# Kernel optimization log

Measured on AMD Instinct MI355X. Metric: run time of the kernel, lower is better.

Reference implementation:

```python
import jax, jax.numpy as jnp
import numpy as np

B, H, S, D = 2, 16, 2048, 128
ALIBI_MAX_BIAS = 8.0


def alibi_bias(seq_len: int, num_heads: int):
    # slopes = 2 ** -(start, 2*start, ..., num_heads*start), start = max_bias / num_heads
    start = ALIBI_MAX_BIAS / num_heads
    slopes = jnp.exp2(-(jnp.arange(1, num_heads + 1, dtype=jnp.float32) * start))  # [H]
    dist = (jnp.arange(seq_len)[None, :] - jnp.arange(seq_len)[:, None]).astype(jnp.float32)  # [S,S] j-i
    return (dist[None, :, :] * slopes[:, None, None])[None]  # [1,H,S,S]


def setup_inputs() -> dict:
    key = jax.random.key(0)
    kq, kk, kv = jax.random.split(key, 3)
    q = jax.random.normal(kq, (B, H, S, D), dtype=jnp.float32)
    k = jax.random.normal(kk, (B, H, S, D), dtype=jnp.float32)
    v = jax.random.normal(kv, (B, H, S, D), dtype=jnp.float32)
    mask = jnp.tril(jnp.ones((S, S), dtype=jnp.int32))[None, None]  # causal [1,1,S,S]
    return {"q": q, "k": k, "v": v, "mask": mask}


def reference(q, k, v, mask):
    dim = q.shape[-1]
    scale = jnp.sqrt(jnp.asarray(dim, dtype=q.dtype))
    alibi = alibi_bias(k.shape[-2], k.shape[-3]).astype(q.dtype)
    mat = jnp.einsum("bhsd,bhtd->bhst", q, k) / scale + alibi  # [B,H,S,S]
    mat = jnp.where(mask == 0, jnp.asarray(-1000000.0, dtype=mat.dtype), mat)
    mat = jax.nn.softmax(mat, axis=-1)
    return jnp.einsum("bhst,bhtd->bhsd", mat, v)
```

## Files before the change

### kernel.cpp

```cpp
#include <hip/hip_runtime.h>
#include <hip/hip_bf16.h>

typedef short s16x8 __attribute__((ext_vector_type(8)));
typedef float f32x16 __attribute__((ext_vector_type(16)));

#define LOG2E 1.44269504088896f

__device__ __forceinline__ unsigned bfpack2(float lo, float hi) {
  unsigned a = (unsigned)__builtin_bit_cast(unsigned short, __float2bfloat16(lo));
  unsigned b = (unsigned)__builtin_bit_cast(unsigned short, __float2bfloat16(hi));
  return a | (b << 16);
}

union U4 { unsigned u[4]; uint4 q; s16x8 v; };

__global__ __launch_bounds__(128)
void prep_kv(const float* __restrict__ Kg, const float* __restrict__ Vg,
             char* __restrict__ tiles) {
  constexpr int S = 2048, Dh = 128;
  const int g  = (int)blockIdx.x;
  const int bh = g >> 6, t = g & 63;
  const size_t base = (size_t)bh * S * Dh + (size_t)(t << 5) * Dh;
  char* out = tiles + ((size_t)g << 14);
  const int tid = (int)threadIdx.x;
  const int lane = tid & 63, half = tid >> 6;
  const int l31 = lane & 31, h5 = lane >> 5;

  {
    const float* krow = Kg + base + (size_t)l31 * Dh;
    #pragma unroll
    for (int i = 0; i < 4; ++i) {
      const int ks = half * 4 + i;
      const float* p = krow + 16 * ks + 8 * h5;
      float4 a = *(const float4*)p;
      float4 b = *(const float4*)(p + 4);
      U4 w;
      w.u[0] = bfpack2(a.x, a.y); w.u[1] = bfpack2(a.z, a.w);
      w.u[2] = bfpack2(b.x, b.y); w.u[3] = bfpack2(b.z, b.w);
      *(uint4*)(out + ks * 1024 + lane * 16) = w.q;
    }
  }
  __shared__ float lds[32][132];
  {
    const int rv = tid >> 2, q4 = tid & 3;
    const float* vrow = Vg + base + (size_t)rv * Dh;
    #pragma unroll
    for (int p = 0; p < 8; ++p)
      *(float4*)(&lds[rv][q4 * 4 + p * 16]) = *(const float4*)(vrow + q4 * 4 + p * 16);
  }
  __syncthreads();
  {
    #pragma unroll
    for (int i = 0; i < 4; ++i) {
      const int gp = half * 4 + i;
      const int ks = gp >> 2, dt = gp & 3;
      const int cv = 2 * ks + h5, d = 32 * dt + l31;
      U4 w;
      #pragma unroll
      for (int u = 0; u < 4; ++u)
        w.u[u] = bfpack2(lds[8 * cv + 2 * u][d], lds[8 * cv + 2 * u + 1][d]);
      *(uint4*)(out + 8192 + gp * 1024 + lane * 16) = w.q;
    }
  }
}

__global__ __launch_bounds__(128, 2)
void attn_alibi(const float* __restrict__ Qg, float* __restrict__ Og,
                const char* __restrict__ tiles) {
  constexpr int S = 2048, Dh = 128;
  const int lid  = (int)blockIdx.x;
  const int xcd  = lid & 7;
  const int r8   = lid >> 3;
  const int bh   = xcd + 8 * (r8 & 3);
  const int qt   = 63 - (r8 >> 2);
  const int head = bh & 15;

  const int tid  = (int)threadIdx.x;
  const int wq   = tid >> 6;
  const int lane = tid & 63, l31 = lane & 31, h5 = lane >> 5;

  const float c1     = 0.08838834764831845f * LOG2E;
  const float slope2 = exp2f(-0.5f * (float)(head + 1)) * LOG2E;

  const char* tb = tiles + (((size_t)bh << 6) << 14);

  float cpat[16];
  #pragma unroll
  for (int r = 0; r < 16; ++r)
    cpat[r] = slope2 * (float)((r & 3) + 8 * (r >> 2) + 4 * h5);

  __shared__ float olds[4][64][17];
  __shared__ float mlds[2][2][32];

  const int iq = (qt << 5) + l31;

  s16x8 qf[8];
  {
    const float* qrow = Qg + (size_t)bh * S * Dh + (size_t)iq * Dh;
    #pragma unroll
    for (int ks = 0; ks < 8; ++ks) {
      const float* p = qrow + 16 * ks + 8 * h5;
      float4 a = *(const float4*)p;
      float4 b = *(const float4*)(p + 4);
      U4 w;
      w.u[0] = bfpack2(a.x, a.y); w.u[1] = bfpack2(a.z, a.w);
      w.u[2] = bfpack2(b.x, b.y); w.u[3] = bfpack2(b.z, b.w);
      qf[ks] = w.v;
    }
  }

  f32x16 oacc[4];
  #pragma unroll
  for (int dt = 0; dt < 4; ++dt)
    #pragma unroll
    for (int r = 0; r < 16; ++r) oacc[dt][r] = 0.0f;
  float m2 = -3.0e38f, lsum = 0.0f;

  const int nt = qt + 1;
  for (int t = wq; t < nt; t += 2) {
    const char* kb = tb + ((size_t)t << 14) + lane * 16;
    s16x8 kf[8], vf[8];
    #pragma unroll
    for (int ks = 0; ks < 8; ++ks)
      kf[ks] = *(const s16x8*)(kb + ks * 1024);
    #pragma unroll
    for (int gp = 0; gp < 8; ++gp)
      vf[gp] = *(const s16x8*)(kb + 8192 + gp * 1024);

    f32x16 sc;
    #pragma unroll
    for (int r = 0; r < 16; ++r) sc[r] = 0.0f;
    __builtin_amdgcn_s_setprio(1);
    #pragma unroll
    for (int ks = 0; ks < 8; ++ks)
      sc = __builtin_amdgcn_mfma_f32_32x32x16_bf16(kf[ks], qf[ks], sc, 0, 0, 0);
    __builtin_amdgcn_s_setprio(0);

    const float sb = slope2 * (float)((t << 5) - iq);
    float mloc = -3.0e38f;
    if (t != qt) {
      #pragma unroll
      for (int r = 0; r < 16; ++r) {
        float v = fmaf(sc[r], c1, sb + cpat[r]);
        sc[r] = v;
        mloc = fmaxf(mloc, v);
      }
    } else {
      #pragma unroll
      for (int r = 0; r < 16; ++r) {
        const float b = sb + cpat[r];
        float v = fmaf(sc[r], c1, b);
        v = (b > 0.0f) ? -3.0e38f : v;
        sc[r] = v;
        mloc = fmaxf(mloc, v);
      }
    }
    mloc = fmaxf(mloc, __shfl_xor(mloc, 32));
    if (!__all(mloc <= m2 + 8.0f)) {
      const float mnew = fmaxf(m2, mloc);
      const float corr = __builtin_amdgcn_exp2f(m2 - mnew);
      m2 = mnew;
      lsum *= corr;
      #pragma unroll
      for (int dt = 0; dt < 4; ++dt)
        #pragma unroll
        for (int r = 0; r < 16; ++r) oacc[dt][r] *= corr;
    }
    float ps = 0.0f;
    #pragma unroll
    for (int r = 0; r < 16; ++r) {
      const float p = __builtin_amdgcn_exp2f(sc[r] - m2);
      sc[r] = p;
      ps += p;
    }
    lsum += ps;

    unsigned pk[4][2];
    #pragma unroll
    for (int rg = 0; rg < 4; ++rg) {
      pk[rg][0] = bfpack2(sc[4 * rg + 0], sc[4 * rg + 1]);
      pk[rg][1] = bfpack2(sc[4 * rg + 2], sc[4 * rg + 3]);
    }

    #pragma unroll
    for (int ks = 0; ks < 2; ++ks) {
      unsigned a0 = pk[2 * ks][0], b0 = pk[2 * ks + 1][0];
      unsigned a1 = pk[2 * ks][1], b1 = pk[2 * ks + 1][1];
      asm("v_permlane32_swap_b32 %0, %1" : "+v"(a0), "+v"(b0));
      asm("v_permlane32_swap_b32 %0, %1" : "+v"(a1), "+v"(b1));
      U4 bf;
      bf.u[0] = a0; bf.u[1] = a1; bf.u[2] = b0; bf.u[3] = b1;
      __builtin_amdgcn_s_setprio(1);
      #pragma unroll
      for (int dt = 0; dt < 4; ++dt)
        oacc[dt] = __builtin_amdgcn_mfma_f32_32x32x16_bf16(
            vf[4 * ks + dt], bf.v, oacc[dt], 0, 0, 0);
      __builtin_amdgcn_s_setprio(0);
    }
  }

  lsum += __shfl_xor(lsum, 32);
  #pragma unroll
  for (int dtL = 0; dtL < 2; ++dtL) {
    const int dt = 2 * (1 - wq) + dtL;
    #pragma unroll
    for (int r = 0; r < 16; ++r) olds[dt][lane][r] = oacc[dt][r];
  }
  mlds[wq][0][l31] = m2;
  mlds[wq][1][l31] = lsum;
  __syncthreads();
  {
    const float pm = mlds[1 - wq][0][l31];
    const float pl = mlds[1 - wq][1][l31];
    const float ms = fmaxf(m2, pm);
    const float so = __builtin_amdgcn_exp2f(m2 - ms);
    const float sp = __builtin_amdgcn_exp2f(pm - ms);
    const float rl = 1.0f / (lsum * so + pl * sp);
    float* orow = Og + (size_t)bh * S * Dh + (size_t)iq * Dh;
    #pragma unroll
    for (int dtL = 0; dtL < 2; ++dtL) {
      const int dt = 2 * wq + dtL;
      #pragma unroll
      for (int rg = 0; rg < 4; ++rg) {
        float4 v;
        v.x = (oacc[dt][4 * rg + 0] * so + olds[dt][lane][4 * rg + 0] * sp) * rl;
        v.y = (oacc[dt][4 * rg + 1] * so + olds[dt][lane][4 * rg + 1] * sp) * rl;
        v.z = (oacc[dt][4 * rg + 2] * so + olds[dt][lane][4 * rg + 2] * sp) * rl;
        v.w = (oacc[dt][4 * rg + 3] * so + olds[dt][lane][4 * rg + 3] * sp) * rl;
        *(float4*)(orow + 32 * dt + 8 * rg + 4 * h5) = v;
      }
    }
  }
}

extern "C" void kernel_launch(void* const* d_in, const int* in_sizes, int n_in,
                              void* d_out, int out_size, void* d_ws, size_t ws_size,
                              hipStream_t stream) {
  (void)in_sizes; (void)n_in; (void)out_size; (void)ws_size;
  const float* q = (const float*)d_in[0];
  const float* k = (const float*)d_in[1];
  const float* v = (const float*)d_in[2];
  float* o = (float*)d_out;
  char* tiles = (char*)d_ws;
  prep_kv<<<dim3(2048), dim3(128), 0, stream>>>(k, v, tiles);
  attn_alibi<<<dim3(2048), dim3(128), 0, stream>>>(q, o, tiles);
}
```

Measured before the change: 104.1 us.

## Pair causal query tiles per block and split KV across four waves

Each block now processes two query tiles in sequence, a short one (pr) and its long mirror (63-pr), so every block does a similar amount of causal work. Blocks use four waves instead of two, striding KV tiles by four, and merge the partial softmax results in two LDS reduction stages. The grid is halved to 1024 blocks of 256 threads. The goal is better load balance and more parallelism per query tile, at the cost of extra barriers, a larger LDS footprint, and fewer resident blocks.

```diff
diff --git a/kernel.cpp b/kernel.cpp
--- a/kernel.cpp
+++ b/kernel.cpp
@@ -64,7 +64,7 @@
   }
 }
 
-__global__ __launch_bounds__(128, 2)
+__global__ __launch_bounds__(256, 2)
 void attn_alibi(const float* __restrict__ Qg, float* __restrict__ Og,
                 const char* __restrict__ tiles) {
   constexpr int S = 2048, Dh = 128;
@@ -72,12 +72,13 @@
   const int xcd  = lid & 7;
   const int r8   = lid >> 3;
   const int bh   = xcd + 8 * (r8 & 3);
-  const int qt   = 63 - (r8 >> 2);
+  const int pr   = r8 >> 2;
   const int head = bh & 15;
 
   const int tid  = (int)threadIdx.x;
   const int wq   = tid >> 6;
   const int lane = tid & 63, l31 = lane & 31, h5 = lane >> 5;
+  const int pair = wq >> 1, hw = wq & 1;
 
   const float c1     = 0.08838834764831845f * LOG2E;
   const float slope2 = exp2f(-0.5f * (float)(head + 1)) * LOG2E;
@@ -89,147 +90,179 @@
   for (int r = 0; r < 16; ++r)
     cpat[r] = slope2 * (float)((r & 3) + 8 * (r >> 2) + 4 * h5);
 
-  __shared__ float olds[4][64][17];
-  __shared__ float mlds[2][2][32];
-
-  const int iq = (qt << 5) + l31;
-
-  s16x8 qf[8];
-  {
-    const float* qrow = Qg + (size_t)bh * S * Dh + (size_t)iq * Dh;
-    #pragma unroll
-    for (int ks = 0; ks < 8; ++ks) {
-      const float* p = qrow + 16 * ks + 8 * h5;
-      float4 a = *(const float4*)p;
-      float4 b = *(const float4*)(p + 4);
-      U4 w;
-      w.u[0] = bfpack2(a.x, a.y); w.u[1] = bfpack2(a.z, a.w);
-      w.u[2] = bfpack2(b.x, b.y); w.u[3] = bfpack2(b.z, b.w);
-      qf[ks] = w.v;
-    }
-  }
-
-  f32x16 oacc[4];
-  #pragma unroll
-  for (int dt = 0; dt < 4; ++dt)
-    #pragma unroll
-    for (int r = 0; r < 16; ++r) oacc[dt][r] = 0.0f;
-  float m2 = -3.0e38f, lsum = 0.0f;
-
-  const int nt = qt + 1;
-  for (int t = wq; t < nt; t += 2) {
-    const char* kb = tb + ((size_t)t << 14) + lane * 16;
-    s16x8 kf[8], vf[8];
-    #pragma unroll
-    for (int ks = 0; ks < 8; ++ks)
-      kf[ks] = *(const s16x8*)(kb + ks * 1024);
-    #pragma unroll
-    for (int gp = 0; gp < 8; ++gp)
-      vf[gp] = *(const s16x8*)(kb + 8192 + gp * 1024);
-
-    f32x16 sc;
-    #pragma unroll
-    for (int r = 0; r < 16; ++r) sc[r] = 0.0f;
-    __builtin_amdgcn_s_setprio(1);
-    #pragma unroll
-    for (int ks = 0; ks < 8; ++ks)
-      sc = __builtin_amdgcn_mfma_f32_32x32x16_bf16(kf[ks], qf[ks], sc, 0, 0, 0);
-    __builtin_amdgcn_s_setprio(0);
-
-    const float sb = slope2 * (float)((t << 5) - iq);
-    float mloc = -3.0e38f;
-    if (t != qt) {
+  __shared__ float olds[2][4][64][17];
+  __shared__ float mlds[4][2][32];
+
+  for (int ph = 0; ph < 2; ++ph) {
+    const int qt = ph ? (63 - pr) : pr;
+    const int iq = (qt << 5) + l31;
+
+    s16x8 qf[8];
+    {
+      const float* qrow = Qg + (size_t)bh * S * Dh + (size_t)iq * Dh;
+      #pragma unroll
+      for (int ks = 0; ks < 8; ++ks) {
+        const float* p = qrow + 16 * ks + 8 * h5;
+        float4 a = *(const float4*)p;
+        float4 b = *(const float4*)(p + 4);
+        U4 w;
+        w.u[0] = bfpack2(a.x, a.y); w.u[1] = bfpack2(a.z, a.w);
+        w.u[2] = bfpack2(b.x, b.y); w.u[3] = bfpack2(b.z, b.w);
+        qf[ks] = w.v;
+      }
+    }
+
+    f32x16 oacc[4];
+    #pragma unroll
+    for (int dt = 0; dt < 4; ++dt)
+      #pragma unroll
+      for (int r = 0; r < 16; ++r) oacc[dt][r] = 0.0f;
+    float m2 = -3.0e38f, lsum = 0.0f;
+
+    const int nt = qt + 1;
+    for (int t = wq; t < nt; t += 4) {
+      const char* kb = tb + ((size_t)t << 14) + lane * 16;
+      s16x8 kf[8], vf[8];
+      #pragma unroll
+      for (int ks = 0; ks < 8; ++ks)
+        kf[ks] = *(const s16x8*)(kb + ks * 1024);
+      #pragma unroll
+      for (int gp = 0; gp < 8; ++gp)
+        vf[gp] = *(const s16x8*)(kb + 8192 + gp * 1024);
+
+      f32x16 sc;
+      #pragma unroll
+      for (int r = 0; r < 16; ++r) sc[r] = 0.0f;
+      __builtin_amdgcn_s_setprio(1);
+      #pragma unroll
+      for (int ks = 0; ks < 8; ++ks)
+        sc = __builtin_amdgcn_mfma_f32_32x32x16_bf16(kf[ks], qf[ks], sc, 0, 0, 0);
+      __builtin_amdgcn_s_setprio(0);
+
+      const float sb = slope2 * (float)((t << 5) - iq);
+      float mloc = -3.0e38f;
+      if (t != qt) {
+        #pragma unroll
+        for (int r = 0; r < 16; ++r) {
+          float v = fmaf(sc[r], c1, sb + cpat[r]);
+          sc[r] = v;
+          mloc = fmaxf(mloc, v);
+        }
+      } else {
+        #pragma unroll
+        for (int r = 0; r < 16; ++r) {
+          const float b = sb + cpat[r];
+          float v = fmaf(sc[r], c1, b);
+          v = (b > 0.0f) ? -3.0e38f : v;
+          sc[r] = v;
+          mloc = fmaxf(mloc, v);
+        }
+      }
+      mloc = fmaxf(mloc, __shfl_xor(mloc, 32));
+      if (!__all(mloc <= m2 + 8.0f)) {
+        const float mnew = fmaxf(m2, mloc);
+        const float corr = __builtin_amdgcn_exp2f(m2 - mnew);
+        m2 = mnew;
+        lsum *= corr;
+        #pragma unroll
+        for (int dt = 0; dt < 4; ++dt)
+          #pragma unroll
+          for (int r = 0; r < 16; ++r) oacc[dt][r] *= corr;
+      }
+      float ps = 0.0f;
       #pragma unroll
       for (int r = 0; r < 16; ++r) {
-        float v = fmaf(sc[r], c1, sb + cpat[r]);
-        sc[r] = v;
-        mloc = fmaxf(mloc, v);
-      }
-    } else {
-      #pragma unroll
-      for (int r = 0; r < 16; ++r) {
-        const float b = sb + cpat[r];
-        float v = fmaf(sc[r], c1, b);
-        v = (b > 0.0f) ? -3.0e38f : v;
-        sc[r] = v;
-        mloc = fmaxf(mloc, v);
-      }
-    }
-    mloc = fmaxf(mloc, __shfl_xor(mloc, 32));
-    if (!__all(mloc <= m2 + 8.0f)) {
-      const float mnew = fmaxf(m2, mloc);
-      const float corr = __builtin_amdgcn_exp2f(m2 - mnew);
-      m2 = mnew;
-      lsum *= corr;
-      #pragma unroll
-      for (int dt = 0; dt < 4; ++dt)
-        #pragma unroll
-        for (int r = 0; r < 16; ++r) oacc[dt][r] *= corr;
-    }
-    float ps = 0.0f;
-    #pragma unroll
-    for (int r = 0; r < 16; ++r) {
-      const float p = __builtin_amdgcn_exp2f(sc[r] - m2);
-      sc[r] = p;
-      ps += p;
-    }
-    lsum += ps;
-
-    unsigned pk[4][2];
-    #pragma unroll
-    for (int rg = 0; rg < 4; ++rg) {
-      pk[rg][0] = bfpack2(sc[4 * rg + 0], sc[4 * rg + 1]);
-      pk[rg][1] = bfpack2(sc[4 * rg + 2], sc[4 * rg + 3]);
-    }
-
-    #pragma unroll
-    for (int ks = 0; ks < 2; ++ks) {
-      unsigned a0 = pk[2 * ks][0], b0 = pk[2 * ks + 1][0];
-      unsigned a1 = pk[2 * ks][1], b1 = pk[2 * ks + 1][1];
-      asm("v_permlane32_swap_b32 %0, %1" : "+v"(a0), "+v"(b0));
-      asm("v_permlane32_swap_b32 %0, %1" : "+v"(a1), "+v"(b1));
-      U4 bf;
-      bf.u[0] = a0; bf.u[1] = a1; bf.u[2] = b0; bf.u[3] = b1;
-      __builtin_amdgcn_s_setprio(1);
-      #pragma unroll
-      for (int dt = 0; dt < 4; ++dt)
-        oacc[dt] = __builtin_amdgcn_mfma_f32_32x32x16_bf16(
-            vf[4 * ks + dt], bf.v, oacc[dt], 0, 0, 0);
-      __builtin_amdgcn_s_setprio(0);
-    }
-  }
-
-  lsum += __shfl_xor(lsum, 32);
-  #pragma unroll
-  for (int dtL = 0; dtL < 2; ++dtL) {
-    const int dt = 2 * (1 - wq) + dtL;
-    #pragma unroll
-    for (int r = 0; r < 16; ++r) olds[dt][lane][r] = oacc[dt][r];
-  }
-  mlds[wq][0][l31] = m2;
-  mlds[wq][1][l31] = lsum;
-  __syncthreads();
-  {
-    const float pm = mlds[1 - wq][0][l31];
-    const float pl = mlds[1 - wq][1][l31];
-    const float ms = fmaxf(m2, pm);
-    const float so = __builtin_amdgcn_exp2f(m2 - ms);
-    const float sp = __builtin_amdgcn_exp2f(pm - ms);
-    const float rl = 1.0f / (lsum * so + pl * sp);
-    float* orow = Og + (size_t)bh * S * Dh + (size_t)iq * Dh;
+        const float p = __builtin_amdgcn_exp2f(sc[r] - m2);
+        sc[r] = p;
+        ps += p;
+      }
+      lsum += ps;
+
+      unsigned pk[4][2];
+      #pragma unroll
+      for (int rg = 0; rg < 4; ++rg) {
+        pk[rg][0] = bfpack2(sc[4 * rg + 0], sc[4 * rg + 1]);
+        pk[rg][1] = bfpack2(sc[4 * rg + 2], sc[4 * rg + 3]);
+      }
+
+      #pragma unroll
+      for (int ks = 0; ks < 2; ++ks) {
+        unsigned a0 = pk[2 * ks][0], b0 = pk[2 * ks + 1][0];
+        unsigned a1 = pk[2 * ks][1], b1 = pk[2 * ks + 1][1];
+        asm("v_permlane32_swap_b32 %0, %1" : "+v"(a0), "+v"(b0));
+        asm("v_permlane32_swap_b32 %0, %1" : "+v"(a1), "+v"(b1));
+        U4 bf;
+        bf.u[0] = a0; bf.u[1] = a1; bf.u[2] = b0; bf.u[3] = b1;
+        __builtin_amdgcn_s_setprio(1);
+        #pragma unroll
+        for (int dt = 0; dt < 4; ++dt)
+          oacc[dt] = __builtin_amdgcn_mfma_f32_32x32x16_bf16(
+              vf[4 * ks + dt], bf.v, oacc[dt], 0, 0, 0);
+        __builtin_amdgcn_s_setprio(0);
+      }
+    }
+
+    lsum += __shfl_xor(lsum, 32);
+
     #pragma unroll
     for (int dtL = 0; dtL < 2; ++dtL) {
-      const int dt = 2 * wq + dtL;
-      #pragma unroll
-      for (int rg = 0; rg < 4; ++rg) {
-        float4 v;
-        v.x = (oacc[dt][4 * rg + 0] * so + olds[dt][lane][4 * rg + 0] * sp) * rl;
-        v.y = (oacc[dt][4 * rg + 1] * so + olds[dt][lane][4 * rg + 1] * sp) * rl;
-        v.z = (oacc[dt][4 * rg + 2] * so + olds[dt][lane][4 * rg + 2] * sp) * rl;
-        v.w = (oacc[dt][4 * rg + 3] * so + olds[dt][lane][4 * rg + 3] * sp) * rl;
-        *(float4*)(orow + 32 * dt + 8 * rg + 4 * h5) = v;
-      }
-    }
+      const int dt = 2 * (1 - hw) + dtL;
+      #pragma unroll
+      for (int r = 0; r < 16; ++r) olds[pair][dt][lane][r] = oacc[dt][r];
+    }
+    mlds[wq][0][l31] = m2;
+    mlds[wq][1][l31] = lsum;
+    __syncthreads();
+    const float pm = mlds[wq ^ 1][0][l31];
+    const float pl = mlds[wq ^ 1][1][l31];
+    const float ms1 = fmaxf(m2, pm);
+    const float so1 = __builtin_amdgcn_exp2f(m2 - ms1);
+    const float sp1 = __builtin_amdgcn_exp2f(pm - ms1);
+    const float l1  = lsum * so1 + pl * sp1;
+    #pragma unroll
+    for (int dtL = 0; dtL < 2; ++dtL) {
+      const int dt = 2 * hw + dtL;
+      #pragma unroll
+      for (int r = 0; r < 16; ++r)
+        oacc[dt][r] = oacc[dt][r] * so1 + olds[pair][dt][lane][r] * sp1;
+    }
+    __syncthreads();
+
+    if (pair == 1) {
+      #pragma unroll
+      for (int dtL = 0; dtL < 2; ++dtL) {
+        const int dt = 2 * hw + dtL;
+        #pragma unroll
+        for (int r = 0; r < 16; ++r)
+          olds[0][dt][lane][r] = oacc[dt][r];
+      }
+      mlds[wq][0][l31] = ms1;
+      mlds[wq][1][l31] = l1;
+    }
+    __syncthreads();
+    if (pair == 0) {
+      const float pm2 = mlds[wq + 2][0][l31];
+      const float pl2 = mlds[wq + 2][1][l31];
+      const float ms2 = fmaxf(ms1, pm2);
+      const float so2 = __builtin_amdgcn_exp2f(ms1 - ms2);
+      const float sp2 = __builtin_amdgcn_exp2f(pm2 - ms2);
+      const float rl  = 1.0f / (l1 * so2 + pl2 * sp2);
+      float* orow = Og + (size_t)bh * S * Dh + (size_t)iq * Dh;
+      #pragma unroll
+      for (int dtL = 0; dtL < 2; ++dtL) {
+        const int dt = 2 * hw + dtL;
+        #pragma unroll
+        for (int rg = 0; rg < 4; ++rg) {
+          float4 v;
+          v.x = (oacc[dt][4 * rg + 0] * so2 + olds[0][dt][lane][4 * rg + 0] * sp2) * rl;
+          v.y = (oacc[dt][4 * rg + 1] * so2 + olds[0][dt][lane][4 * rg + 1] * sp2) * rl;
+          v.z = (oacc[dt][4 * rg + 2] * so2 + olds[0][dt][lane][4 * rg + 2] * sp2) * rl;
+          v.w = (oacc[dt][4 * rg + 3] * so2 + olds[0][dt][lane][4 * rg + 3] * sp2) * rl;
+          *(float4*)(orow + 32 * dt + 8 * rg + 4 * h5) = v;
+        }
+      }
+    }
+    __syncthreads();
   }
 }
 
@@ -243,5 +276,5 @@
   float* o = (float*)d_out;
   char* tiles = (char*)d_ws;
   prep_kv<<<dim3(2048), dim3(128), 0, stream>>>(k, v, tiles);
-  attn_alibi<<<dim3(2048), dim3(128), 0, stream>>>(q, o, tiles);
-}
+  attn_alibi<<<dim3(1024), dim3(256), 0, stream>>>(q, o, tiles);
+}
```

Result: slower. 151.4 us (+45.5%).

## Share double-buffered K/V tiles in LDS across four query-tile waves

Applied to the files above, without the earlier changes.

Each block of four waves now owns four consecutive 32-row query tiles. The block cooperatively stages K/V tiles into double-buffered shared memory, and every wave reuses them from LDS. Previously each wave pair split the key tiles of a single query tile and merged partial softmax states through LDS; now each wave processes all keys for its own query tile, which removes the cross-wave merge. This cuts redundant global/L2 reads of K/V, but adds a barrier per tile, leaves waves idle on the diagonal because of causal imbalance within a block, and reduces the grid to 512 blocks.

```diff
diff --git a/kernel.cpp b/kernel.cpp
--- a/kernel.cpp
+++ b/kernel.cpp
@@ -64,20 +64,23 @@
   }
 }
 
-__global__ __launch_bounds__(128, 2)
+__global__ __launch_bounds__(256, 2)
 void attn_alibi(const float* __restrict__ Qg, float* __restrict__ Og,
                 const char* __restrict__ tiles) {
   constexpr int S = 2048, Dh = 128;
   const int lid  = (int)blockIdx.x;
   const int xcd  = lid & 7;
-  const int r8   = lid >> 3;
-  const int bh   = xcd + 8 * (r8 & 3);
-  const int qt   = 63 - (r8 >> 2);
+  const int b2   = (lid >> 3) & 3;
+  const int bh   = xcd + 8 * b2;
+  const int qb   = 15 - (lid >> 5);
   const int head = bh & 15;
 
   const int tid  = (int)threadIdx.x;
   const int wq   = tid >> 6;
   const int lane = tid & 63, l31 = lane & 31, h5 = lane >> 5;
+
+  const int qtw  = 4 * qb + wq;
+  const int iq   = (qtw << 5) + l31;
 
   const float c1     = 0.08838834764831845f * LOG2E;
   const float slope2 = exp2f(-0.5f * (float)(head + 1)) * LOG2E;
@@ -89,10 +92,7 @@
   for (int r = 0; r < 16; ++r)
     cpat[r] = slope2 * (float)((r & 3) + 8 * (r >> 2) + 4 * h5);
 
-  __shared__ float olds[4][64][17];
-  __shared__ float mlds[2][2][32];
-
-  const int iq = (qt << 5) + l31;
+  __shared__ __align__(16) char smem[32768];
 
   s16x8 qf[8];
   {
@@ -116,16 +116,35 @@
     for (int r = 0; r < 16; ++r) oacc[dt][r] = 0.0f;
   float m2 = -3.0e38f, lsum = 0.0f;
 
-  const int nt = qt + 1;
-  for (int t = wq; t < nt; t += 2) {
-    const char* kb = tb + ((size_t)t << 14) + lane * 16;
+#define STAGE(buf, tt) do {                                                   \
+    const char* src_ = tb + ((size_t)(tt) << 14) + wq * 4096 + lane * 16;     \
+    char* dst_ = smem + ((buf) << 14) + wq * 4096 + lane * 16;                \
+    uint4 r0_ = *(const uint4*)(src_);                                        \
+    uint4 r1_ = *(const uint4*)(src_ + 1024);                                 \
+    uint4 r2_ = *(const uint4*)(src_ + 2048);                                 \
+    uint4 r3_ = *(const uint4*)(src_ + 3072);                                 \
+    *(uint4*)(dst_)        = r0_;                                             \
+    *(uint4*)(dst_ + 1024) = r1_;                                             \
+    *(uint4*)(dst_ + 2048) = r2_;                                             \
+    *(uint4*)(dst_ + 3072) = r3_;                                             \
+  } while (0)
+
+  const int nt = 4 * qb + 4;
+  STAGE(0, 0);
+
+  for (int t = 0; t < nt; ++t) {
+    __syncthreads();
+    if (t + 1 < nt) STAGE((t + 1) & 1, t + 1);
+    if (t > qtw) continue;
+    const char* kbuf = smem + ((t & 1) << 14);
+
     s16x8 kf[8], vf[8];
     #pragma unroll
     for (int ks = 0; ks < 8; ++ks)
-      kf[ks] = *(const s16x8*)(kb + ks * 1024);
+      kf[ks] = *(const s16x8*)(kbuf + ks * 1024 + lane * 16);
     #pragma unroll
     for (int gp = 0; gp < 8; ++gp)
-      vf[gp] = *(const s16x8*)(kb + 8192 + gp * 1024);
+      vf[gp] = *(const s16x8*)(kbuf + 8192 + gp * 1024 + lane * 16);
 
     f32x16 sc;
     #pragma unroll
@@ -138,7 +157,7 @@
 
     const float sb = slope2 * (float)((t << 5) - iq);
     float mloc = -3.0e38f;
-    if (t != qt) {
+    if (t != qtw) {
       #pragma unroll
       for (int r = 0; r < 16; ++r) {
         float v = fmaf(sc[r], c1, sb + cpat[r]);
@@ -198,39 +217,22 @@
       __builtin_amdgcn_s_setprio(0);
     }
   }
+#undef STAGE
 
   lsum += __shfl_xor(lsum, 32);
+  const float rl = 1.0f / lsum;
+  float* orow = Og + (size_t)bh * S * Dh + (size_t)iq * Dh;
   #pragma unroll
-  for (int dtL = 0; dtL < 2; ++dtL) {
-    const int dt = 2 * (1 - wq) + dtL;
-    #pragma unroll
-    for (int r = 0; r < 16; ++r) olds[dt][lane][r] = oacc[dt][r];
-  }
-  mlds[wq][0][l31] = m2;
-  mlds[wq][1][l31] = lsum;
-  __syncthreads();
-  {
-    const float pm = mlds[1 - wq][0][l31];
-    const float pl = mlds[1 - wq][1][l31];
-    const float ms = fmaxf(m2, pm);
-    const float so = __builtin_amdgcn_exp2f(m2 - ms);
-    const float sp = __builtin_amdgcn_exp2f(pm - ms);
-    const float rl = 1.0f / (lsum * so + pl * sp);
-    float* orow = Og + (size_t)bh * S * Dh + (size_t)iq * Dh;
-    #pragma unroll
-    for (int dtL = 0; dtL < 2; ++dtL) {
-      const int dt = 2 * wq + dtL;
-      #pragma unroll
-      for (int rg = 0; rg < 4; ++rg) {
-        float4 v;
-        v.x = (oacc[dt][4 * rg + 0] * so + olds[dt][lane][4 * rg + 0] * sp) * rl;
-        v.y = (oacc[dt][4 * rg + 1] * so + olds[dt][lane][4 * rg + 1] * sp) * rl;
-        v.z = (oacc[dt][4 * rg + 2] * so + olds[dt][lane][4 * rg + 2] * sp) * rl;
-        v.w = (oacc[dt][4 * rg + 3] * so + olds[dt][lane][4 * rg + 3] * sp) * rl;
-        *(float4*)(orow + 32 * dt + 8 * rg + 4 * h5) = v;
-      }
-    }
-  }
+  for (int dt = 0; dt < 4; ++dt)
+    #pragma unroll
+    for (int rg = 0; rg < 4; ++rg) {
+      float4 v;
+      v.x = oacc[dt][4 * rg + 0] * rl;
+      v.y = oacc[dt][4 * rg + 1] * rl;
+      v.z = oacc[dt][4 * rg + 2] * rl;
+      v.w = oacc[dt][4 * rg + 3] * rl;
+      *(float4*)(orow + 32 * dt + 8 * rg + 4 * h5) = v;
+    }
 }
 
 extern "C" void kernel_launch(void* const* d_in, const int* in_sizes, int n_in,
@@ -243,5 +245,5 @@
   float* o = (float*)d_out;
   char* tiles = (char*)d_ws;
   prep_kv<<<dim3(2048), dim3(128), 0, stream>>>(k, v, tiles);
-  attn_alibi<<<dim3(2048), dim3(128), 0, stream>>>(q, o, tiles);
-}
+  attn_alibi<<<dim3(512), dim3(256), 0, stream>>>(q, o, tiles);
+}
```

New measurement: 101.4 us. 1.03x faster.
